# Performance work log

Measured on AMD Instinct MI355X. Metric: run time of the kernel, lower is better.

Reference implementation:

```python
import jax, jax.numpy as jnp
import numpy as np

N_BASIS = 16
CUTOFF = 5.0
S3 = 3.0 ** 0.5


def _cg_121():
    # Real Clebsch-Gordan for 1o x 2e -> 1o built from the equivariant map
    # (v, T) -> T @ v where T is the traceless symmetric matrix encoded by the
    # 5 real l=2 components (e3nn y-principal convention). Normalized to unit
    # Frobenius norm (wigner-3j-like normalization).
    s15 = np.sqrt(15.0); s5 = np.sqrt(5.0)
    C = np.zeros((3, 3, 5))
    for j in range(5):
        c = np.zeros(5); c[j] = 1.0
        T = np.zeros((3, 3))
        T[0, 2] = T[2, 0] = c[0] / s15
        T[0, 1] = T[1, 0] = c[1] / s15
        T[1, 2] = T[2, 1] = c[3] / s15
        Tyy = 2.0 * c[2] / (3.0 * s5)
        T[1, 1] = Tyy
        T[2, 2] = -Tyy / 2.0 + c[4] / s15
        T[0, 0] = -Tyy / 2.0 - c[4] / s15
        C[:, :, j] = T
    C /= np.linalg.norm(C)
    return jnp.asarray(C, dtype=jnp.float32)


def _sph(n):
    # component-normalized real spherical harmonics l=0,1,2 of unit vectors n [E,3]
    x, y, z = n[:, 0], n[:, 1], n[:, 2]
    Y0 = jnp.ones_like(x)
    Y1 = S3 * n  # [E,3]
    s15 = 15.0 ** 0.5; s5 = 5.0 ** 0.5
    Y2 = jnp.stack([s15 * x * z, s15 * x * y, 0.5 * s5 * (3 * y * y - 1.0),
                    s15 * y * z, 0.5 * s15 * (z * z - x * x)], axis=-1)  # [E,5]
    return Y0, Y1, Y2


def _tfn_forward(x, pos, W1, W2, edge_index, cg121):
    row, col = edge_index[0], edge_index[1]
    E = row.shape[0]
    N = pos.shape[0]
    ev = pos[row] - pos[col]                         # [E,3]
    d = jnp.sqrt(jnp.sum(ev * ev, axis=-1) + 1e-12)  # [E]
    n = ev / d[:, None]
    # Gaussian radial basis, 16 centers on [0, cutoff]
    mu = jnp.linspace(0.0, CUTOFF, N_BASIS)
    delta = CUTOFF / (N_BASIS - 1)
    rbf = jnp.exp(-((d[:, None] - mu) ** 2) / (2.0 * delta * delta))  # [E,16]
    # normalized 2-layer MLP -> per-edge TP weights [E, 576]
    h = jax.nn.relu((rbf @ W1) / jnp.sqrt(16.0))
    w = (h @ W2) / jnp.sqrt(64.0)
    Y0, Y1, Y2 = _sph(n)
    ss = jnp.stack([Y0, Y0], axis=-1)   # [E,2]  2x0e
    sv = jnp.stack([Y1, Y1], axis=1)    # [E,2,3] 2x1o
    st = Y2                              # [E,5]  1x2e
    xs = x[row, :8]                      # [E,8]  8x0e
    xv = x[row, 8:].reshape(E, 8, 3)     # [E,8,3] 8x1o
    wA = w[:, 0:128].reshape(E, 8, 2, 8)
    wB = w[:, 128:256].reshape(E, 8, 2, 8)
    wC = w[:, 256:384].reshape(E, 8, 2, 8)
    wD = w[:, 384:512].reshape(E, 8, 2, 8)
    wE = w[:, 512:576].reshape(E, 8, 8)
    a0 = 1.0 / jnp.sqrt(32.0)            # sqrt(2*0+1)/sqrt(fan_in=32)
    a1 = jnp.sqrt(3.0) / jnp.sqrt(40.0)  # sqrt(2*1+1)/sqrt(fan_in=40)
    out_s = a0 * (jnp.einsum('euvw,eu,ev->ew', wA, xs, ss)
                  + jnp.einsum('euvw,eui,evi->ew', wB, xv, sv) / S3)
    out_v = a1 * (jnp.einsum('euvw,eu,evk->ewk', wC, xs, sv) / S3
                  + jnp.einsum('euvw,euk,ev->ewk', wD, xv, ss) / S3
                  + jnp.einsum('euw,eui,ej,kij->ewk', wE, xv, st, cg121))
    out = jnp.concatenate([out_s, out_v.reshape(E, 24)], axis=-1)  # [E,32]
    y = jax.ops.segment_sum(out, row, num_segments=N)              # [N,32]
    # gate: silu on scalar (l=0) channels only
    return jnp.concatenate([jax.nn.silu(y[:, :8]), y[:, 8:]], axis=-1)


def setup_inputs() -> dict:
    key = jax.random.key(0)
    k1, k2, k3, k4, k5 = jax.random.split(key, 5)
    N, E = 25000, 400000
    x = jax.random.normal(k1, (N, 32), dtype=jnp.float32)
    pos = jax.random.normal(k2, (N, 3), dtype=jnp.float32)
    edge_index = jax.random.randint(k3, (2, E), 0, N, dtype=jnp.int64 if jax.config.read('jax_enable_x64') else jnp.int32)
    W1 = jax.random.normal(k4, (16, 64), dtype=jnp.float32)
    W2 = jax.random.normal(k5, (64, 576), dtype=jnp.float32)
    return {"x": x, "pos": pos, "edge_index": edge_index, "W1": W1, "W2": W2}


def reference(x, pos, edge_index, W1, W2):
    cg121 = _cg_121()
    return _tfn_forward(x, pos, W1, W2, edge_index, cg121)
```

## Files before the change

kernel.cpp:

```cpp
#include <hip/hip_runtime.h>
#include <hip/hip_fp16.h>


#define INV_S3  0.5773502691896258f
#define A0S     0.1767766952966369f
#define A1S     0.27386127875258306f
#define S15     3.872983346207417f
#define S5      2.23606797749979f
#define INV_S10 0.31622776601683794f
#define INV_S30 0.18257418583505536f

#define TBL   2048
#define DMAX  8.0f
#define CAP   64

typedef _Float16 half8 __attribute__((ext_vector_type(8)));
typedef _Float16 half2v __attribute__((ext_vector_type(2)));

__global__ __launch_bounds__(256) void prep_all(
    const float* __restrict__ W1, const float* __restrict__ W2,
    const int* __restrict__ ei, const float* __restrict__ pos,
    _Float16* __restrict__ T, int* __restrict__ cnt,
    float4* __restrict__ srec, int E) {

    __shared__ float hs[4][64];
    int tid = threadIdx.x;
    int wv = tid >> 6, lane = tid & 63;
    int j = blockIdx.x * 4 + wv;

    float hv = 0.f;
    if (j < TBL) {
        float d = (float)j * (DMAX / (float)(TBL - 1));
        float acc = 0.f;
#pragma unroll
        for (int i = 0; i < 16; ++i) {
            float t = d - (float)i * (1.0f / 3.0f);
            float r = __expf(-4.5f * t * t);
            acc = fmaf(r, W1[i * 64 + lane], acc);
        }
        hv = fmaxf(acc, 0.f) * 0.25f;
    }
    hs[wv][lane] = hv;
    __syncthreads();

    if (j < TBL) {
        int u = lane >> 3, wo = lane & 7;
        int b0 = u * 16 + wo;
        int b4 = 512 + u * 8 + wo;
        float a0 = 0.f, a1 = 0.f, a2 = 0.f, a3 = 0.f, a4 = 0.f;
#pragma unroll 4
        for (int k = 0; k < 64; ++k) {
            float hk = hs[wv][k];
            const float* Wk = W2 + k * 576;
            a0 = fmaf(hk, Wk[b0]       + Wk[b0 + 8],       a0);
            a1 = fmaf(hk, Wk[128 + b0] + Wk[128 + b0 + 8], a1);
            a2 = fmaf(hk, Wk[256 + b0] + Wk[256 + b0 + 8], a2);
            a3 = fmaf(hk, Wk[384 + b0] + Wk[384 + b0 + 8], a3);
            a4 = fmaf(hk, Wk[b4], a4);
        }
        _Float16* Tr = T + (size_t)j * 320;
        int base = u * 16 + wo * 2;
        Tr[base]           = (_Float16)a0;
        Tr[base + 1]       = (_Float16)a1;
        Tr[128 + base]     = (_Float16)a2;
        Tr[128 + base + 1] = (_Float16)a3;
        Tr[256 + u * 8 + wo] = (_Float16)a4;
    }

    int gtid = blockIdx.x * 256 + tid;
    int gsz = gridDim.x * 256;
    for (int e = gtid; e < E; e += gsz) {
        int row = ei[e];
        int col = ei[E + e];
        float ax = pos[3 * row + 0] - pos[3 * col + 0];
        float ay = pos[3 * row + 1] - pos[3 * col + 1];
        float az = pos[3 * row + 2] - pos[3 * col + 2];
        float d2 = ax * ax + ay * ay + az * az + 1e-12f;
        float invd = rsqrtf(d2);
        float dd = d2 * invd;
        int p = atomicAdd(&cnt[row], 1);
        if (p < CAP) {
            float4 r;
            r.x = ax * invd;
            r.y = ay * invd;
            r.z = az * invd;
            r.w = dd;
            srec[(size_t)row * CAP + p] = r;
        }
    }
}

__global__ __launch_bounds__(64) void tfn_node(
    const float* __restrict__ x, const float4* __restrict__ srec,
    const int* __restrict__ cnt, const _Float16* __restrict__ T,
    float* __restrict__ y, int N) {

    int lane = threadIdx.x & 63;
    int n = blockIdx.x;
    if (n >= N) return;

    int g = lane >> 3;
    int u = lane & 7;
    int kc = cnt[n];
    if (kc > CAP) kc = CAP;
    const float4* recs = srec + (size_t)n * CAP;

    const float* xr = x + (size_t)n * 32;
    float xu  = xr[u];
    float xv0 = xr[8 + 3 * u + 0];
    float xv1 = xr[8 + 3 * u + 1];
    float xv2 = xr[8 + 3 * u + 2];
    _Float16 xuh = (_Float16)xu;
    _Float16 p30 = (_Float16)(xv0 * INV_S3);
    _Float16 p31 = (_Float16)(xv1 * INV_S3);
    _Float16 p32 = (_Float16)(xv2 * INV_S3);

    float V[32];
#pragma unroll
    for (int z = 0; z < 32; ++z) V[z] = 0.f;

    int rounds = (kc + 7) >> 3;
    float4 rec = make_float4(0.f, 0.f, 0.f, 0.f);
    if (rounds > 0) rec = recs[g];
    for (int rd = 0; rd < rounds; ++rd) {
        float4 cur = rec;
        int slot = rd * 8 + g;
        if (rd + 1 < rounds) rec = recs[slot + 8];
        if (slot < kc) {
            float nx = cur.x, ny = cur.y, nz = cur.z;
            float dd = cur.w;

            float fj = dd * ((float)(TBL - 1) / DMAX);
            int j0 = (int)fj;
            j0 = min(j0, TBL - 2);
            float tf = fminf(fj - (float)j0, 1.0f);
            _Float16 th = (_Float16)tf;

            const _Float16* Ar = T + (size_t)j0 * 320;
            const _Float16* Au = Ar + u * 16;
            half8 A01a = *(const half8*)(Au);
            half8 A01b = *(const half8*)(Au + 8);
            half8 A23a = *(const half8*)(Au + 128);
            half8 A23b = *(const half8*)(Au + 136);
            half8 A4   = *(const half8*)(Ar + 256 + u * 8);
            half8 B01a = *(const half8*)(Au + 320);
            half8 B01b = *(const half8*)(Au + 328);
            half8 B23a = *(const half8*)(Au + 448);
            half8 B23b = *(const half8*)(Au + 456);
            half8 B4   = *(const half8*)(Ar + 576 + u * 8);

            float qu = xv0 * nx + xv1 * ny + xv2 * nz;
            float Y22 = 0.5f * S5 * (3.f * ny * ny - 1.f);
            float Y24 = 0.5f * S15 * (nz * nz - nx * nx);
            float M00 = -Y22 * INV_S30 - Y24 * INV_S10;
            float M11 = 2.f * Y22 * INV_S30;
            float M22 = -Y22 * INV_S30 + Y24 * INV_S10;
            float M01 = (S15 * nx * ny) * INV_S10;
            float M02 = (S15 * nx * nz) * INV_S10;
            float M12 = (S15 * ny * nz) * INV_S10;
            float m0 = M00 * xv0 + M01 * xv1 + M02 * xv2;
            float m1 = M01 * xv0 + M11 * xv1 + M12 * xv2;
            float m2 = M02 * xv0 + M12 * xv1 + M22 * xv2;

            half2v xq;  xq.x = xuh;  xq.y = (_Float16)qu;
            half2v c0;  c0.x = (_Float16)(xu * nx);  c0.y = p30;
            half2v c1;  c1.x = (_Float16)(xu * ny);  c1.y = p31;
            half2v c2;  c2.x = (_Float16)(xu * nz);  c2.y = p32;

            half8 w01a, w01b, w23a, w23b, w4l;
#pragma unroll
            for (int z = 0; z < 8; ++z) {
                w01a[z] = A01a[z] + (B01a[z] - A01a[z]) * th;
                w01b[z] = A01b[z] + (B01b[z] - A01b[z]) * th;
                w23a[z] = A23a[z] + (B23a[z] - A23a[z]) * th;
                w23b[z] = A23b[z] + (B23b[z] - A23b[z]) * th;
                w4l[z]  = A4[z]   + (B4[z]   - A4[z])   * th;
            }

#pragma unroll
            for (int z = 0; z < 4; ++z) {
                half2v pa; pa.x = w01a[2 * z]; pa.y = w01a[2 * z + 1];
                V[z] = __builtin_amdgcn_fdot2(pa, xq, V[z], false);
                half2v pb; pb.x = w01b[2 * z]; pb.y = w01b[2 * z + 1];
                V[4 + z] = __builtin_amdgcn_fdot2(pb, xq, V[4 + z], false);
            }

#pragma unroll
            for (int z = 0; z < 4; ++z) {
                half2v pa; pa.x = w23a[2 * z]; pa.y = w23a[2 * z + 1];
                int b = 8 + 3 * z;
                V[b]     = __builtin_amdgcn_fdot2(pa, c0, V[b],     false);
                V[b + 1] = __builtin_amdgcn_fdot2(pa, c1, V[b + 1], false);
                V[b + 2] = __builtin_amdgcn_fdot2(pa, c2, V[b + 2], false);
                half2v pb; pb.x = w23b[2 * z]; pb.y = w23b[2 * z + 1];
                int b2 = 8 + 3 * (z + 4);
                V[b2]     = __builtin_amdgcn_fdot2(pb, c0, V[b2],     false);
                V[b2 + 1] = __builtin_amdgcn_fdot2(pb, c1, V[b2 + 1], false);
                V[b2 + 2] = __builtin_amdgcn_fdot2(pb, c2, V[b2 + 2], false);
            }

#pragma unroll
            for (int z = 0; z < 8; ++z) {
                float we = (float)w4l[z];
                V[8 + 3 * z]  = fmaf(m0, we, V[8 + 3 * z]);
                V[9 + 3 * z]  = fmaf(m1, we, V[9 + 3 * z]);
                V[10 + 3 * z] = fmaf(m2, we, V[10 + 3 * z]);
            }
        }
    }

#pragma unroll
    for (int h = 16; h >= 1; h >>= 1) {
        bool hi = (lane & h) != 0;
#pragma unroll
        for (int k = 0; k < h; ++k) {
            float lo = V[k], up = V[k + h];
            float keep = hi ? up : lo;
            float send = hi ? lo : up;
            V[k] = keep + __shfl_xor(send, h, 64);
        }
    }
    V[0] += __shfl_xor(V[0], 32, 64);

    if (lane < 32) {
        float v = V[0] * 0.125f * (lane < 8 ? A0S : A1S);
        if (lane < 8) v = v / (1.0f + __expf(-v));
        y[(size_t)n * 32 + lane] = v;
    }
}

extern "C" void kernel_launch(void* const* d_in, const int* in_sizes, int n_in,
                              void* d_out, int out_size, void* d_ws, size_t ws_size,
                              hipStream_t stream) {
    const float* x   = (const float*)d_in[0];
    const float* pos = (const float*)d_in[1];
    const int*   ei  = (const int*)d_in[2];
    const float* W1  = (const float*)d_in[3];
    const float* W2  = (const float*)d_in[4];
    int N = in_sizes[1] / 3;
    int E = in_sizes[2] / 2;

    char* ws = (char*)d_ws;
    size_t off = 0;
    _Float16* T    = (_Float16*)(ws + off); off += (size_t)TBL * 320 * 2;
    int*      cnt  = (int*)(ws + off);      off += (size_t)N * 4;
    float4*   srec = (float4*)(ws + off);   off += (size_t)N * CAP * 16;

    float* y = (float*)d_out;

    hipMemsetAsync(cnt, 0, (size_t)N * 4, stream);
    hipLaunchKernelGGL(prep_all, dim3(2048), dim3(256), 0, stream,
                       W1, W2, ei, pos, T, cnt, srec, E);
    hipLaunchKernelGGL(tfn_node, dim3(N), dim3(64), 0, stream,
                       x, srec, cnt, T, y, N);
}
```

Before: 134.1 us.

## Make node kernel persistent with grid-stride loop and prefetch next node

The per-node kernel now runs as a fixed grid of 4096 blocks with two waves each, and each wave strides over nodes instead of one block per node. While processing the current node, it prefetches the next node's count, features and first edge record so their latency overlaps with compute. This cuts block launch overhead and hides per-node startup loads, but fixes the degree of parallelism and adds register pressure from the prefetched values.

```diff
diff --git a/kernel.cpp b/kernel.cpp
--- a/kernel.cpp
+++ b/kernel.cpp
@@ -13,6 +13,7 @@
 #define TBL   2048
 #define DMAX  8.0f
 #define CAP   64
+#define NBLK  4096
 
 typedef _Float16 half8 __attribute__((ext_vector_type(8)));
 typedef _Float16 half2v __attribute__((ext_vector_type(2)));
@@ -90,142 +91,167 @@
     }
 }
 
-__global__ __launch_bounds__(64) void tfn_node(
+__global__ __launch_bounds__(128) void tfn_node(
     const float* __restrict__ x, const float4* __restrict__ srec,
     const int* __restrict__ cnt, const _Float16* __restrict__ T,
     float* __restrict__ y, int N) {
 
-    int lane = threadIdx.x & 63;
-    int n = blockIdx.x;
-    if (n >= N) return;
-
+    int wv = threadIdx.x >> 6, lane = threadIdx.x & 63;
     int g = lane >> 3;
     int u = lane & 7;
+    const int wstride = NBLK * 2;
+
+    int n = blockIdx.x * 2 + wv;
+    if (n >= N) return;
+
     int kc = cnt[n];
-    if (kc > CAP) kc = CAP;
-    const float4* recs = srec + (size_t)n * CAP;
-
-    const float* xr = x + (size_t)n * 32;
-    float xu  = xr[u];
-    float xv0 = xr[8 + 3 * u + 0];
-    float xv1 = xr[8 + 3 * u + 1];
-    float xv2 = xr[8 + 3 * u + 2];
-    _Float16 xuh = (_Float16)xu;
-    _Float16 p30 = (_Float16)(xv0 * INV_S3);
-    _Float16 p31 = (_Float16)(xv1 * INV_S3);
-    _Float16 p32 = (_Float16)(xv2 * INV_S3);
-
-    float V[32];
-#pragma unroll
-    for (int z = 0; z < 32; ++z) V[z] = 0.f;
-
-    int rounds = (kc + 7) >> 3;
-    float4 rec = make_float4(0.f, 0.f, 0.f, 0.f);
-    if (rounds > 0) rec = recs[g];
-    for (int rd = 0; rd < rounds; ++rd) {
-        float4 cur = rec;
-        int slot = rd * 8 + g;
-        if (rd + 1 < rounds) rec = recs[slot + 8];
-        if (slot < kc) {
-            float nx = cur.x, ny = cur.y, nz = cur.z;
-            float dd = cur.w;
-
-            float fj = dd * ((float)(TBL - 1) / DMAX);
-            int j0 = (int)fj;
-            j0 = min(j0, TBL - 2);
-            float tf = fminf(fj - (float)j0, 1.0f);
-            _Float16 th = (_Float16)tf;
-
-            const _Float16* Ar = T + (size_t)j0 * 320;
-            const _Float16* Au = Ar + u * 16;
-            half8 A01a = *(const half8*)(Au);
-            half8 A01b = *(const half8*)(Au + 8);
-            half8 A23a = *(const half8*)(Au + 128);
-            half8 A23b = *(const half8*)(Au + 136);
-            half8 A4   = *(const half8*)(Ar + 256 + u * 8);
-            half8 B01a = *(const half8*)(Au + 320);
-            half8 B01b = *(const half8*)(Au + 328);
-            half8 B23a = *(const half8*)(Au + 448);
-            half8 B23b = *(const half8*)(Au + 456);
-            half8 B4   = *(const half8*)(Ar + 576 + u * 8);
-
-            float qu = xv0 * nx + xv1 * ny + xv2 * nz;
-            float Y22 = 0.5f * S5 * (3.f * ny * ny - 1.f);
-            float Y24 = 0.5f * S15 * (nz * nz - nx * nx);
-            float M00 = -Y22 * INV_S30 - Y24 * INV_S10;
-            float M11 = 2.f * Y22 * INV_S30;
-            float M22 = -Y22 * INV_S30 + Y24 * INV_S10;
-            float M01 = (S15 * nx * ny) * INV_S10;
-            float M02 = (S15 * nx * nz) * INV_S10;
-            float M12 = (S15 * ny * nz) * INV_S10;
-            float m0 = M00 * xv0 + M01 * xv1 + M02 * xv2;
-            float m1 = M01 * xv0 + M11 * xv1 + M12 * xv2;
-            float m2 = M02 * xv0 + M12 * xv1 + M22 * xv2;
-
-            half2v xq;  xq.x = xuh;  xq.y = (_Float16)qu;
-            half2v c0;  c0.x = (_Float16)(xu * nx);  c0.y = p30;
-            half2v c1;  c1.x = (_Float16)(xu * ny);  c1.y = p31;
-            half2v c2;  c2.x = (_Float16)(xu * nz);  c2.y = p32;
-
-            half8 w01a, w01b, w23a, w23b, w4l;
-#pragma unroll
-            for (int z = 0; z < 8; ++z) {
-                w01a[z] = A01a[z] + (B01a[z] - A01a[z]) * th;
-                w01b[z] = A01b[z] + (B01b[z] - A01b[z]) * th;
-                w23a[z] = A23a[z] + (B23a[z] - A23a[z]) * th;
-                w23b[z] = A23b[z] + (B23b[z] - A23b[z]) * th;
-                w4l[z]  = A4[z]   + (B4[z]   - A4[z])   * th;
+    {
+    }
+    const float* xr0 = x + (size_t)n * 32;
+    float xu  = xr0[u];
+    float xv0 = xr0[8 + 3 * u + 0];
+    float xv1 = xr0[8 + 3 * u + 1];
+    float xv2 = xr0[8 + 3 * u + 2];
+    float4 rec0 = srec[(size_t)n * CAP + g];
+
+    while (true) {
+        int n2 = n + wstride;
+        int kc2 = 0;
+        float xu_2 = 0.f, xv0_2 = 0.f, xv1_2 = 0.f, xv2_2 = 0.f;
+        float4 rec0_2 = rec0;
+        if (n2 < N) {
+            kc2 = cnt[n2];
+            const float* xr2 = x + (size_t)n2 * 32;
+            xu_2  = xr2[u];
+            xv0_2 = xr2[8 + 3 * u + 0];
+            xv1_2 = xr2[8 + 3 * u + 1];
+            xv2_2 = xr2[8 + 3 * u + 2];
+            rec0_2 = srec[(size_t)n2 * CAP + g];
+        }
+
+        if (kc > CAP) kc = CAP;
+        const float4* recs = srec + (size_t)n * CAP;
+        _Float16 xuh = (_Float16)xu;
+        _Float16 p30 = (_Float16)(xv0 * INV_S3);
+        _Float16 p31 = (_Float16)(xv1 * INV_S3);
+        _Float16 p32 = (_Float16)(xv2 * INV_S3);
+
+        float V[32];
+#pragma unroll
+        for (int z = 0; z < 32; ++z) V[z] = 0.f;
+
+        int rounds = (kc + 7) >> 3;
+        float4 rec = rec0;
+        for (int rd = 0; rd < rounds; ++rd) {
+            float4 cur = rec;
+            int slot = rd * 8 + g;
+            if (rd + 1 < rounds) rec = recs[slot + 8];
+            if (slot < kc) {
+                float nx = cur.x, ny = cur.y, nz = cur.z;
+                float dd = cur.w;
+
+                float fj = dd * ((float)(TBL - 1) / DMAX);
+                int j0 = (int)fj;
+                j0 = min(j0, TBL - 2);
+                float tf = fminf(fj - (float)j0, 1.0f);
+                _Float16 th = (_Float16)tf;
+
+                const _Float16* Ar = T + (size_t)j0 * 320;
+                const _Float16* Au = Ar + u * 16;
+                half8 A01a = *(const half8*)(Au);
+                half8 A01b = *(const half8*)(Au + 8);
+                half8 A23a = *(const half8*)(Au + 128);
+                half8 A23b = *(const half8*)(Au + 136);
+                half8 A4   = *(const half8*)(Ar + 256 + u * 8);
+                half8 B01a = *(const half8*)(Au + 320);
+                half8 B01b = *(const half8*)(Au + 328);
+                half8 B23a = *(const half8*)(Au + 448);
+                half8 B23b = *(const half8*)(Au + 456);
+                half8 B4   = *(const half8*)(Ar + 576 + u * 8);
+
+                float qu = xv0 * nx + xv1 * ny + xv2 * nz;
+                float Y22 = 0.5f * S5 * (3.f * ny * ny - 1.f);
+                float Y24 = 0.5f * S15 * (nz * nz - nx * nx);
+                float M00 = -Y22 * INV_S30 - Y24 * INV_S10;
+                float M11 = 2.f * Y22 * INV_S30;
+                float M22 = -Y22 * INV_S30 + Y24 * INV_S10;
+                float M01 = (S15 * nx * ny) * INV_S10;
+                float M02 = (S15 * nx * nz) * INV_S10;
+                float M12 = (S15 * ny * nz) * INV_S10;
+                float m0 = M00 * xv0 + M01 * xv1 + M02 * xv2;
+                float m1 = M01 * xv0 + M11 * xv1 + M12 * xv2;
+                float m2 = M02 * xv0 + M12 * xv1 + M22 * xv2;
+
+                half2v xq;  xq.x = xuh;  xq.y = (_Float16)qu;
+                half2v c0;  c0.x = (_Float16)(xu * nx);  c0.y = p30;
+                half2v c1;  c1.x = (_Float16)(xu * ny);  c1.y = p31;
+                half2v c2;  c2.x = (_Float16)(xu * nz);  c2.y = p32;
+
+                half8 w01a, w01b, w23a, w23b, w4l;
+#pragma unroll
+                for (int z = 0; z < 8; ++z) {
+                    w01a[z] = A01a[z] + (B01a[z] - A01a[z]) * th;
+                    w01b[z] = A01b[z] + (B01b[z] - A01b[z]) * th;
+                    w23a[z] = A23a[z] + (B23a[z] - A23a[z]) * th;
+                    w23b[z] = A23b[z] + (B23b[z] - A23b[z]) * th;
+                    w4l[z]  = A4[z]   + (B4[z]   - A4[z])   * th;
+                }
+
+#pragma unroll
+                for (int z = 0; z < 4; ++z) {
+                    half2v pa; pa.x = w01a[2 * z]; pa.y = w01a[2 * z + 1];
+                    V[z] = __builtin_amdgcn_fdot2(pa, xq, V[z], false);
+                    half2v pb; pb.x = w01b[2 * z]; pb.y = w01b[2 * z + 1];
+                    V[4 + z] = __builtin_amdgcn_fdot2(pb, xq, V[4 + z], false);
+                }
+
+#pragma unroll
+                for (int z = 0; z < 4; ++z) {
+                    half2v pa; pa.x = w23a[2 * z]; pa.y = w23a[2 * z + 1];
+                    int b = 8 + 3 * z;
+                    V[b]     = __builtin_amdgcn_fdot2(pa, c0, V[b],     false);
+                    V[b + 1] = __builtin_amdgcn_fdot2(pa, c1, V[b + 1], false);
+                    V[b + 2] = __builtin_amdgcn_fdot2(pa, c2, V[b + 2], false);
+                    half2v pb; pb.x = w23b[2 * z]; pb.y = w23b[2 * z + 1];
+                    int b2 = 8 + 3 * (z + 4);
+                    V[b2]     = __builtin_amdgcn_fdot2(pb, c0, V[b2],     false);
+                    V[b2 + 1] = __builtin_amdgcn_fdot2(pb, c1, V[b2 + 1], false);
+                    V[b2 + 2] = __builtin_amdgcn_fdot2(pb, c2, V[b2 + 2], false);
+                }
+
+#pragma unroll
+                for (int z = 0; z < 8; ++z) {
+                    float we = (float)w4l[z];
+                    V[8 + 3 * z]  = fmaf(m0, we, V[8 + 3 * z]);
+                    V[9 + 3 * z]  = fmaf(m1, we, V[9 + 3 * z]);
+                    V[10 + 3 * z] = fmaf(m2, we, V[10 + 3 * z]);
+                }
             }
-
-#pragma unroll
-            for (int z = 0; z < 4; ++z) {
-                half2v pa; pa.x = w01a[2 * z]; pa.y = w01a[2 * z + 1];
-                V[z] = __builtin_amdgcn_fdot2(pa, xq, V[z], false);
-                half2v pb; pb.x = w01b[2 * z]; pb.y = w01b[2 * z + 1];
-                V[4 + z] = __builtin_amdgcn_fdot2(pb, xq, V[4 + z], false);
+        }
+
+#pragma unroll
+        for (int h = 16; h >= 1; h >>= 1) {
+            bool hi = (lane & h) != 0;
+#pragma unroll
+            for (int k = 0; k < h; ++k) {
+                float lo = V[k], up = V[k + h];
+                float keep = hi ? up : lo;
+                float send = hi ? lo : up;
+                V[k] = keep + __shfl_xor(send, h, 64);
             }
-
-#pragma unroll
-            for (int z = 0; z < 4; ++z) {
-                half2v pa; pa.x = w23a[2 * z]; pa.y = w23a[2 * z + 1];
-                int b = 8 + 3 * z;
-                V[b]     = __builtin_amdgcn_fdot2(pa, c0, V[b],     false);
-                V[b + 1] = __builtin_amdgcn_fdot2(pa, c1, V[b + 1], false);
-                V[b + 2] = __builtin_amdgcn_fdot2(pa, c2, V[b + 2], false);
-                half2v pb; pb.x = w23b[2 * z]; pb.y = w23b[2 * z + 1];
-                int b2 = 8 + 3 * (z + 4);
-                V[b2]     = __builtin_amdgcn_fdot2(pb, c0, V[b2],     false);
-                V[b2 + 1] = __builtin_amdgcn_fdot2(pb, c1, V[b2 + 1], false);
-                V[b2 + 2] = __builtin_amdgcn_fdot2(pb, c2, V[b2 + 2], false);
-            }
-
-#pragma unroll
-            for (int z = 0; z < 8; ++z) {
-                float we = (float)w4l[z];
-                V[8 + 3 * z]  = fmaf(m0, we, V[8 + 3 * z]);
-                V[9 + 3 * z]  = fmaf(m1, we, V[9 + 3 * z]);
-                V[10 + 3 * z] = fmaf(m2, we, V[10 + 3 * z]);
-            }
-        }
-    }
-
-#pragma unroll
-    for (int h = 16; h >= 1; h >>= 1) {
-        bool hi = (lane & h) != 0;
-#pragma unroll
-        for (int k = 0; k < h; ++k) {
-            float lo = V[k], up = V[k + h];
-            float keep = hi ? up : lo;
-            float send = hi ? lo : up;
-            V[k] = keep + __shfl_xor(send, h, 64);
-        }
-    }
-    V[0] += __shfl_xor(V[0], 32, 64);
-
-    if (lane < 32) {
-        float v = V[0] * 0.125f * (lane < 8 ? A0S : A1S);
-        if (lane < 8) v = v / (1.0f + __expf(-v));
-        y[(size_t)n * 32 + lane] = v;
+        }
+        V[0] += __shfl_xor(V[0], 32, 64);
+
+        if (lane < 32) {
+            float v = V[0] * 0.125f * (lane < 8 ? A0S : A1S);
+            if (lane < 8) v = v / (1.0f + __expf(-v));
+            y[(size_t)n * 32 + lane] = v;
+        }
+
+        if (n2 >= N) break;
+        n = n2; kc = kc2;
+        xu = xu_2; xv0 = xv0_2; xv1 = xv1_2; xv2 = xv2_2;
+        rec0 = rec0_2;
     }
 }
 
@@ -251,6 +277,6 @@
     hipMemsetAsync(cnt, 0, (size_t)N * 4, stream);
     hipLaunchKernelGGL(prep_all, dim3(2048), dim3(256), 0, stream,
                        W1, W2, ei, pos, T, cnt, srec, E);
-    hipLaunchKernelGGL(tfn_node, dim3(N), dim3(64), 0, stream,
+    hipLaunchKernelGGL(tfn_node, dim3(NBLK), dim3(128), 0, stream,
                        x, srec, cnt, T, y, N);
 }
```

Result: slower. 140.4 us (+4.7%).

## Split node-centric kernel into edge-parallel compute plus per-node gather-sum

Applied to the files above, without the earlier changes.

Replaces the one-wavefront-per-node kernel, where lanes idle whenever a node has a ragged edge count, with an edge-parallel kernel. Each group of 8 lanes handles one edge, reduces it across the u lanes with shuffles, and writes a 32-channel fp16 result per edge. A third kernel then gathers those per-edge outputs through a per-node edge-index list and applies the scaling and SiLU gate. This balances work across edges but adds an E×32 fp16 intermediate buffer, an extra launch, an extra in-edge reduction per edge, and fp16 rounding of the per-edge outputs.

```diff
diff --git a/kernel.cpp b/kernel.cpp
--- a/kernel.cpp
+++ b/kernel.cpp
@@ -15,13 +15,13 @@
 #define CAP   64
 
 typedef _Float16 half8 __attribute__((ext_vector_type(8)));
+typedef _Float16 half4v __attribute__((ext_vector_type(4)));
 typedef _Float16 half2v __attribute__((ext_vector_type(2)));
 
 __global__ __launch_bounds__(256) void prep_all(
     const float* __restrict__ W1, const float* __restrict__ W2,
-    const int* __restrict__ ei, const float* __restrict__ pos,
-    _Float16* __restrict__ T, int* __restrict__ cnt,
-    float4* __restrict__ srec, int E) {
+    const int* __restrict__ ei, _Float16* __restrict__ T,
+    int* __restrict__ cnt, int* __restrict__ scol, int E) {
 
     __shared__ float hs[4][64];
     int tid = threadIdx.x;
@@ -71,70 +71,50 @@
     int gsz = gridDim.x * 256;
     for (int e = gtid; e < E; e += gsz) {
         int row = ei[e];
-        int col = ei[E + e];
-        float ax = pos[3 * row + 0] - pos[3 * col + 0];
-        float ay = pos[3 * row + 1] - pos[3 * col + 1];
-        float az = pos[3 * row + 2] - pos[3 * col + 2];
-        float d2 = ax * ax + ay * ay + az * az + 1e-12f;
-        float invd = rsqrtf(d2);
-        float dd = d2 * invd;
         int p = atomicAdd(&cnt[row], 1);
-        if (p < CAP) {
-            float4 r;
-            r.x = ax * invd;
-            r.y = ay * invd;
-            r.z = az * invd;
-            r.w = dd;
-            srec[(size_t)row * CAP + p] = r;
-        }
-    }
-}
-
-__global__ __launch_bounds__(64) void tfn_node(
-    const float* __restrict__ x, const float4* __restrict__ srec,
-    const int* __restrict__ cnt, const _Float16* __restrict__ T,
-    float* __restrict__ y, int N) {
-
-    int lane = threadIdx.x & 63;
-    int n = blockIdx.x;
-    if (n >= N) return;
-
-    int g = lane >> 3;
-    int u = lane & 7;
-    int kc = cnt[n];
-    if (kc > CAP) kc = CAP;
-    const float4* recs = srec + (size_t)n * CAP;
-
-    const float* xr = x + (size_t)n * 32;
-    float xu  = xr[u];
-    float xv0 = xr[8 + 3 * u + 0];
-    float xv1 = xr[8 + 3 * u + 1];
-    float xv2 = xr[8 + 3 * u + 2];
-    _Float16 xuh = (_Float16)xu;
-    _Float16 p30 = (_Float16)(xv0 * INV_S3);
-    _Float16 p31 = (_Float16)(xv1 * INV_S3);
-    _Float16 p32 = (_Float16)(xv2 * INV_S3);
-
-    float V[32];
-#pragma unroll
-    for (int z = 0; z < 32; ++z) V[z] = 0.f;
-
-    int rounds = (kc + 7) >> 3;
-    float4 rec = make_float4(0.f, 0.f, 0.f, 0.f);
-    if (rounds > 0) rec = recs[g];
-    for (int rd = 0; rd < rounds; ++rd) {
-        float4 cur = rec;
-        int slot = rd * 8 + g;
-        if (rd + 1 < rounds) rec = recs[slot + 8];
-        if (slot < kc) {
-            float nx = cur.x, ny = cur.y, nz = cur.z;
-            float dd = cur.w;
+        if (p < CAP) scol[(size_t)row * CAP + p] = e;
+    }
+}
+
+__global__ __launch_bounds__(256) void tfn_edge(
+    const float* __restrict__ x, const float* __restrict__ pos,
+    const int* __restrict__ ei, const _Float16* __restrict__ T,
+    _Float16* __restrict__ eout, int E) {
+
+    int tid = threadIdx.x;
+    int lane = tid & 63;
+    int g = lane >> 3, u = lane & 7;
+    int wg = blockIdx.x * 4 + (tid >> 6);
+    const int wstride = gridDim.x * 4;
+
+    for (int base = wg; base * 8 < E; base += wstride) {
+        int e = base * 8 + g;
+        if (e < E) {
+            int row = ei[e];
+            int col = ei[E + e];
+            float ax = pos[3 * row + 0] - pos[3 * col + 0];
+            float ay = pos[3 * row + 1] - pos[3 * col + 1];
+            float az = pos[3 * row + 2] - pos[3 * col + 2];
+            float d2 = ax * ax + ay * ay + az * az + 1e-12f;
+            float invd = rsqrtf(d2);
+            float dd = d2 * invd;
+            float nx = ax * invd, ny = ay * invd, nz = az * invd;
 
             float fj = dd * ((float)(TBL - 1) / DMAX);
             int j0 = (int)fj;
             j0 = min(j0, TBL - 2);
             float tf = fminf(fj - (float)j0, 1.0f);
             _Float16 th = (_Float16)tf;
+
+            const float* xr = x + (size_t)row * 32;
+            float xu  = xr[u];
+            float xv0 = xr[8 + 3 * u + 0];
+            float xv1 = xr[8 + 3 * u + 1];
+            float xv2 = xr[8 + 3 * u + 2];
+            _Float16 xuh = (_Float16)xu;
+            _Float16 p30 = (_Float16)(xv0 * INV_S3);
+            _Float16 p31 = (_Float16)(xv1 * INV_S3);
+            _Float16 p32 = (_Float16)(xv2 * INV_S3);
 
             const _Float16* Ar = T + (size_t)j0 * 320;
             const _Float16* Au = Ar + u * 16;
@@ -149,6 +129,10 @@
             half8 B23b = *(const half8*)(Au + 456);
             half8 B4   = *(const half8*)(Ar + 576 + u * 8);
 
+            float V[32];
+#pragma unroll
+            for (int z = 0; z < 32; ++z) V[z] = 0.f;
+
             float qu = xv0 * nx + xv1 * ny + xv2 * nz;
             float Y22 = 0.5f * S5 * (3.f * ny * ny - 1.f);
             float Y24 = 0.5f * S15 * (nz * nz - nx * nx);
@@ -206,26 +190,64 @@
                 V[9 + 3 * z]  = fmaf(m1, we, V[9 + 3 * z]);
                 V[10 + 3 * z] = fmaf(m2, we, V[10 + 3 * z]);
             }
-        }
-    }
-
-#pragma unroll
-    for (int h = 16; h >= 1; h >>= 1) {
-        bool hi = (lane & h) != 0;
-#pragma unroll
-        for (int k = 0; k < h; ++k) {
-            float lo = V[k], up = V[k + h];
-            float keep = hi ? up : lo;
-            float send = hi ? lo : up;
-            V[k] = keep + __shfl_xor(send, h, 64);
-        }
-    }
-    V[0] += __shfl_xor(V[0], 32, 64);
-
-    if (lane < 32) {
-        float v = V[0] * 0.125f * (lane < 8 ? A0S : A1S);
-        if (lane < 8) v = v / (1.0f + __expf(-v));
-        y[(size_t)n * 32 + lane] = v;
+
+#pragma unroll
+            for (int k = 0; k < 16; ++k) {
+                bool hi = (u & 4) != 0;
+                float lo = V[k], up = V[k + 16];
+                float keep = hi ? up : lo, send = hi ? lo : up;
+                V[k] = keep + __shfl_xor(send, 4, 64);
+            }
+#pragma unroll
+            for (int k = 0; k < 8; ++k) {
+                bool hi = (u & 2) != 0;
+                float lo = V[k], up = V[k + 8];
+                float keep = hi ? up : lo, send = hi ? lo : up;
+                V[k] = keep + __shfl_xor(send, 2, 64);
+            }
+#pragma unroll
+            for (int k = 0; k < 4; ++k) {
+                bool hi = (u & 1) != 0;
+                float lo = V[k], up = V[k + 4];
+                float keep = hi ? up : lo, send = hi ? lo : up;
+                V[k] = keep + __shfl_xor(send, 1, 64);
+            }
+
+            half4v ov;
+#pragma unroll
+            for (int k = 0; k < 4; ++k) ov[k] = (_Float16)V[k];
+            *(half4v*)(eout + (size_t)e * 32 + 4 * u) = ov;
+        }
+    }
+}
+
+__global__ __launch_bounds__(256) void tfn_sum(
+    const _Float16* __restrict__ eout, const int* __restrict__ scol,
+    const int* __restrict__ cnt, float* __restrict__ y, int N) {
+
+    int tid = threadIdx.x;
+    int lane = tid & 63;
+    int c = lane & 31, p = lane >> 5;
+    int wg = blockIdx.x * 4 + (tid >> 6);
+    const int wstride = gridDim.x * 4;
+
+    for (int n = wg; n < N; n += wstride) {
+        int kc = cnt[n];
+        if (kc > CAP) kc = CAP;
+        const int* sc = scol + (size_t)n * CAP;
+
+        float acc = 0.f;
+        for (int s = p; s < kc; s += 2) {
+            int e = sc[s];
+            acc += (float)eout[(size_t)e * 32 + c];
+        }
+        acc += __shfl_xor(acc, 32, 64);
+
+        if (lane < 32) {
+            float v = acc * 0.125f * (c < 8 ? A0S : A1S);
+            if (c < 8) v = v / (1.0f + __expf(-v));
+            y[(size_t)n * 32 + lane] = v;
+        }
     }
 }
 
@@ -244,13 +266,16 @@
     size_t off = 0;
     _Float16* T    = (_Float16*)(ws + off); off += (size_t)TBL * 320 * 2;
     int*      cnt  = (int*)(ws + off);      off += (size_t)N * 4;
-    float4*   srec = (float4*)(ws + off);   off += (size_t)N * CAP * 16;
+    int*      scol = (int*)(ws + off);      off += (size_t)N * CAP * 4;
+    _Float16* eout = (_Float16*)(ws + off); off += (size_t)E * 32 * 2;
 
     float* y = (float*)d_out;
 
     hipMemsetAsync(cnt, 0, (size_t)N * 4, stream);
     hipLaunchKernelGGL(prep_all, dim3(2048), dim3(256), 0, stream,
-                       W1, W2, ei, pos, T, cnt, srec, E);
-    hipLaunchKernelGGL(tfn_node, dim3(N), dim3(64), 0, stream,
-                       x, srec, cnt, T, y, N);
-}
+                       W1, W2, ei, T, cnt, scol, E);
+    hipLaunchKernelGGL(tfn_edge, dim3(4096), dim3(256), 0, stream,
+                       x, pos, ei, T, eout, E);
+    hipLaunchKernelGGL(tfn_sum, dim3(2048), dim3(256), 0, stream,
+                       eout, scol, cnt, y, N);
+}
```

Result: slower. 159.5 us (+19.0%).

## Double-buffer per-edge weight table rows into LDS via async global_load_lds

Applied to the files above, without the earlier changes.

Replaces the direct per-lane half8 global loads of the interpolated weight-table rows with asynchronous global_load_lds transfers into a double-buffered shared memory area. The loads for the next round are issued before the current round is computed, and the edge record two rounds ahead is prefetched. The aim is to hide table-gather latency behind the FMA and dot work. In exchange it uses 20 KB of LDS per 64-thread block, which can lower occupancy, and it waits with a full vmcnt(0) at the start of every round.

```diff
diff --git a/kernel.cpp b/kernel.cpp
--- a/kernel.cpp
+++ b/kernel.cpp
@@ -90,17 +90,43 @@
     }
 }
 
+
+#define GL16(GP, LP)                                                        \
+    __builtin_amdgcn_global_load_lds(                                       \
+        (const __attribute__((address_space(1))) unsigned int*)(GP),        \
+        (__attribute__((address_space(3))) unsigned int*)(LP), 16, 0, 0)
+
+#define ISSUE(J0N, BUF) {                                                   \
+    const char* rb_ = (const char*)T + (size_t)(J0N) * 640;                 \
+    char* lb_ = (char*)lbuf[BUF];                                           \
+    GL16(rb_ + o0,        lb_);                                             \
+    GL16(rb_ + o0 + 16,   lb_ + 1024);                                      \
+    GL16(rb_ + o0 + 256,  lb_ + 2048);                                      \
+    GL16(rb_ + o0 + 272,  lb_ + 3072);                                      \
+    GL16(rb_ + o4,        lb_ + 4096);                                      \
+    GL16(rb_ + o0 + 640,  lb_ + 5120);                                      \
+    GL16(rb_ + o0 + 656,  lb_ + 6144);                                      \
+    GL16(rb_ + o0 + 896,  lb_ + 7168);                                      \
+    GL16(rb_ + o0 + 912,  lb_ + 8192);                                      \
+    GL16(rb_ + o4 + 640,  lb_ + 9216); }
+
+#define CLAMPJ(W) max(min((int)((W) * ((float)(TBL - 1) / DMAX)), TBL - 2), 0)
+
 __global__ __launch_bounds__(64) void tfn_node(
     const float* __restrict__ x, const float4* __restrict__ srec,
     const int* __restrict__ cnt, const _Float16* __restrict__ T,
     float* __restrict__ y, int N) {
 
+    __shared__ __align__(16) char lbuf[2][10240];
+
     int lane = threadIdx.x & 63;
     int n = blockIdx.x;
     if (n >= N) return;
 
     int g = lane >> 3;
     int u = lane & 7;
+    int o0 = u * 32;
+    int o4 = 512 + u * 16;
     int kc = cnt[n];
     if (kc > CAP) kc = CAP;
     const float4* recs = srec + (size_t)n * CAP;
@@ -120,92 +146,101 @@
     for (int z = 0; z < 32; ++z) V[z] = 0.f;
 
     int rounds = (kc + 7) >> 3;
-    float4 rec = make_float4(0.f, 0.f, 0.f, 0.f);
-    if (rounds > 0) rec = recs[g];
-    for (int rd = 0; rd < rounds; ++rd) {
-        float4 cur = rec;
-        int slot = rd * 8 + g;
-        if (rd + 1 < rounds) rec = recs[slot + 8];
-        if (slot < kc) {
-            float nx = cur.x, ny = cur.y, nz = cur.z;
-            float dd = cur.w;
-
-            float fj = dd * ((float)(TBL - 1) / DMAX);
-            int j0 = (int)fj;
-            j0 = min(j0, TBL - 2);
-            float tf = fminf(fj - (float)j0, 1.0f);
-            _Float16 th = (_Float16)tf;
-
-            const _Float16* Ar = T + (size_t)j0 * 320;
-            const _Float16* Au = Ar + u * 16;
-            half8 A01a = *(const half8*)(Au);
-            half8 A01b = *(const half8*)(Au + 8);
-            half8 A23a = *(const half8*)(Au + 128);
-            half8 A23b = *(const half8*)(Au + 136);
-            half8 A4   = *(const half8*)(Ar + 256 + u * 8);
-            half8 B01a = *(const half8*)(Au + 320);
-            half8 B01b = *(const half8*)(Au + 328);
-            half8 B23a = *(const half8*)(Au + 448);
-            half8 B23b = *(const half8*)(Au + 456);
-            half8 B4   = *(const half8*)(Ar + 576 + u * 8);
-
-            float qu = xv0 * nx + xv1 * ny + xv2 * nz;
-            float Y22 = 0.5f * S5 * (3.f * ny * ny - 1.f);
-            float Y24 = 0.5f * S15 * (nz * nz - nx * nx);
-            float M00 = -Y22 * INV_S30 - Y24 * INV_S10;
-            float M11 = 2.f * Y22 * INV_S30;
-            float M22 = -Y22 * INV_S30 + Y24 * INV_S10;
-            float M01 = (S15 * nx * ny) * INV_S10;
-            float M02 = (S15 * nx * nz) * INV_S10;
-            float M12 = (S15 * ny * nz) * INV_S10;
-            float m0 = M00 * xv0 + M01 * xv1 + M02 * xv2;
-            float m1 = M01 * xv0 + M11 * xv1 + M12 * xv2;
-            float m2 = M02 * xv0 + M12 * xv1 + M22 * xv2;
-
-            half2v xq;  xq.x = xuh;  xq.y = (_Float16)qu;
-            half2v c0;  c0.x = (_Float16)(xu * nx);  c0.y = p30;
-            half2v c1;  c1.x = (_Float16)(xu * ny);  c1.y = p31;
-            half2v c2;  c2.x = (_Float16)(xu * nz);  c2.y = p32;
-
-            half8 w01a, w01b, w23a, w23b, w4l;
-#pragma unroll
-            for (int z = 0; z < 8; ++z) {
-                w01a[z] = A01a[z] + (B01a[z] - A01a[z]) * th;
-                w01b[z] = A01b[z] + (B01b[z] - A01b[z]) * th;
-                w23a[z] = A23a[z] + (B23a[z] - A23a[z]) * th;
-                w23b[z] = A23b[z] + (B23b[z] - A23b[z]) * th;
-                w4l[z]  = A4[z]   + (B4[z]   - A4[z])   * th;
+    if (rounds > 0) {
+        float4 rc = recs[g];
+        float4 rn = rc;
+        if (rounds > 1) rn = recs[8 + g];
+        ISSUE(CLAMPJ(rc.w), 0);
+
+        for (int rd = 0; rd < rounds; ++rd) {
+            asm volatile("s_waitcnt vmcnt(0)" ::: "memory");
+            __builtin_amdgcn_sched_barrier(0);
+
+            if (rd + 1 < rounds) { ISSUE(CLAMPJ(rn.w), (rd + 1) & 1); }
+            float4 rn2 = rn;
+            if (rd + 2 < rounds) rn2 = recs[(rd + 2) * 8 + g];
+
+            const char* lb = (const char*)lbuf[rd & 1] + lane * 16;
+            half8 A01a = *(const half8*)(lb);
+            half8 A01b = *(const half8*)(lb + 1024);
+            half8 A23a = *(const half8*)(lb + 2048);
+            half8 A23b = *(const half8*)(lb + 3072);
+            half8 A4   = *(const half8*)(lb + 4096);
+            half8 B01a = *(const half8*)(lb + 5120);
+            half8 B01b = *(const half8*)(lb + 6144);
+            half8 B23a = *(const half8*)(lb + 7168);
+            half8 B23b = *(const half8*)(lb + 8192);
+            half8 B4   = *(const half8*)(lb + 9216);
+
+            int slot = rd * 8 + g;
+            if (slot < kc) {
+                float nx = rc.x, ny = rc.y, nz = rc.z;
+                float fj = rc.w * ((float)(TBL - 1) / DMAX);
+                int j0c = min((int)fj, TBL - 2);
+                float tf = fminf(fj - (float)j0c, 1.0f);
+                _Float16 th = (_Float16)tf;
+
+                float qu = xv0 * nx + xv1 * ny + xv2 * nz;
+                float Y22 = 0.5f * S5 * (3.f * ny * ny - 1.f);
+                float Y24 = 0.5f * S15 * (nz * nz - nx * nx);
+                float M00 = -Y22 * INV_S30 - Y24 * INV_S10;
+                float M11 = 2.f * Y22 * INV_S30;
+                float M22 = -Y22 * INV_S30 + Y24 * INV_S10;
+                float M01 = (S15 * nx * ny) * INV_S10;
+                float M02 = (S15 * nx * nz) * INV_S10;
+                float M12 = (S15 * ny * nz) * INV_S10;
+                float m0 = M00 * xv0 + M01 * xv1 + M02 * xv2;
+                float m1 = M01 * xv0 + M11 * xv1 + M12 * xv2;
+                float m2 = M02 * xv0 + M12 * xv1 + M22 * xv2;
+
+                half2v xq;  xq.x = xuh;  xq.y = (_Float16)qu;
+                half2v c0;  c0.x = (_Float16)(xu * nx);  c0.y = p30;
+                half2v c1;  c1.x = (_Float16)(xu * ny);  c1.y = p31;
+                half2v c2;  c2.x = (_Float16)(xu * nz);  c2.y = p32;
+
+                half8 w01a, w01b, w23a, w23b, w4l;
+#pragma unroll
+                for (int z = 0; z < 8; ++z) {
+                    w01a[z] = A01a[z] + (B01a[z] - A01a[z]) * th;
+                    w01b[z] = A01b[z] + (B01b[z] - A01b[z]) * th;
+                    w23a[z] = A23a[z] + (B23a[z] - A23a[z]) * th;
+                    w23b[z] = A23b[z] + (B23b[z] - A23b[z]) * th;
+                    w4l[z]  = A4[z]   + (B4[z]   - A4[z])   * th;
+                }
+
+#pragma unroll
+                for (int z = 0; z < 4; ++z) {
+                    half2v pa; pa.x = w01a[2 * z]; pa.y = w01a[2 * z + 1];
+                    V[z] = __builtin_amdgcn_fdot2(pa, xq, V[z], false);
+                    half2v pb; pb.x = w01b[2 * z]; pb.y = w01b[2 * z + 1];
+                    V[4 + z] = __builtin_amdgcn_fdot2(pb, xq, V[4 + z], false);
+                }
+
+#pragma unroll
+                for (int z = 0; z < 4; ++z) {
+                    half2v pa; pa.x = w23a[2 * z]; pa.y = w23a[2 * z + 1];
+                    int b = 8 + 3 * z;
+                    V[b]     = __builtin_amdgcn_fdot2(pa, c0, V[b],     false);
+                    V[b + 1] = __builtin_amdgcn_fdot2(pa, c1, V[b + 1], false);
+                    V[b + 2] = __builtin_amdgcn_fdot2(pa, c2, V[b + 2], false);
+                    half2v pb; pb.x = w23b[2 * z]; pb.y = w23b[2 * z + 1];
+                    int b2 = 8 + 3 * (z + 4);
+                    V[b2]     = __builtin_amdgcn_fdot2(pb, c0, V[b2],     false);
+                    V[b2 + 1] = __builtin_amdgcn_fdot2(pb, c1, V[b2 + 1], false);
+                    V[b2 + 2] = __builtin_amdgcn_fdot2(pb, c2, V[b2 + 2], false);
+                }
+
+#pragma unroll
+                for (int z = 0; z < 8; ++z) {
+                    float we = (float)w4l[z];
+                    V[8 + 3 * z]  = fmaf(m0, we, V[8 + 3 * z]);
+                    V[9 + 3 * z]  = fmaf(m1, we, V[9 + 3 * z]);
+                    V[10 + 3 * z] = fmaf(m2, we, V[10 + 3 * z]);
+                }
             }
 
-#pragma unroll
-            for (int z = 0; z < 4; ++z) {
-                half2v pa; pa.x = w01a[2 * z]; pa.y = w01a[2 * z + 1];
-                V[z] = __builtin_amdgcn_fdot2(pa, xq, V[z], false);
-                half2v pb; pb.x = w01b[2 * z]; pb.y = w01b[2 * z + 1];
-                V[4 + z] = __builtin_amdgcn_fdot2(pb, xq, V[4 + z], false);
-            }
-
-#pragma unroll
-            for (int z = 0; z < 4; ++z) {
-                half2v pa; pa.x = w23a[2 * z]; pa.y = w23a[2 * z + 1];
-                int b = 8 + 3 * z;
-                V[b]     = __builtin_amdgcn_fdot2(pa, c0, V[b],     false);
-                V[b + 1] = __builtin_amdgcn_fdot2(pa, c1, V[b + 1], false);
-                V[b + 2] = __builtin_amdgcn_fdot2(pa, c2, V[b + 2], false);
-                half2v pb; pb.x = w23b[2 * z]; pb.y = w23b[2 * z + 1];
-                int b2 = 8 + 3 * (z + 4);
-                V[b2]     = __builtin_amdgcn_fdot2(pb, c0, V[b2],     false);
-                V[b2 + 1] = __builtin_amdgcn_fdot2(pb, c1, V[b2 + 1], false);
-                V[b2 + 2] = __builtin_amdgcn_fdot2(pb, c2, V[b2 + 2], false);
-            }
-
-#pragma unroll
-            for (int z = 0; z < 8; ++z) {
-                float we = (float)w4l[z];
-                V[8 + 3 * z]  = fmaf(m0, we, V[8 + 3 * z]);
-                V[9 + 3 * z]  = fmaf(m1, we, V[9 + 3 * z]);
-                V[10 + 3 * z] = fmaf(m2, we, V[10 + 3 * z]);
-            }
+            rc = rn;
+            rn = rn2;
         }
     }
 
```

Measured after the change: 146.8 us. 1.09x slower.
